# Kernel tuning notes

Hardware: AMD Instinct MI355X
Metric: run time of the kernel (lower is better)

Reference implementation:

```python
import jax, jax.numpy as jnp
import numpy as np

SEQ_LEN, BATCH, INPUT_SIZE, HIDDEN = 512, 64, 256, 512


def setup_inputs() -> dict:
    key = jax.random.key(0)
    ks = jax.random.split(key, 5)
    s_in = 1.0 / np.sqrt(INPUT_SIZE)
    s_h = 1.0 / np.sqrt(HIDDEN)
    x = jax.random.normal(ks[0], (SEQ_LEN, BATCH, INPUT_SIZE), dtype=jnp.float32)
    # gate order: f, i, o, c  (matches the torch module's lin_W*/lin_U*)
    Wx = jax.random.uniform(ks[1], (4, HIDDEN, INPUT_SIZE), jnp.float32, -s_in, s_in)
    bx = jax.random.uniform(ks[2], (4, HIDDEN), jnp.float32, -s_in, s_in)
    Wh = jax.random.uniform(ks[3], (4, HIDDEN, HIDDEN), jnp.float32, -s_h, s_h)
    bh = jax.random.uniform(ks[4], (4, HIDDEN), jnp.float32, -s_h, s_h)
    return {"x": x, "Wx": Wx, "bx": bx, "Wh": Wh, "bh": bh}


def reference(x, Wx, bx, Wh, bh):
    # x: [T, B, I]; Wx: [4, H, I]; Wh: [4, H, H]; biases: [4, H] (gate order f,i,o,c)
    T, B, _ = x.shape
    H = Wh.shape[-1]
    # Precompute input projections for all timesteps (batched GEMM): [T, 4, B, H]
    gx = jnp.einsum('tbi,ghi->tgbh', x, Wx) + bx[:, None, :]

    def step(carry, gx_t):
        h_prev, c_prev = carry
        gh = jnp.einsum('bh,gkh->gbk', h_prev, Wh) + bh[:, None, :]  # [4, B, H]
        g = gx_t + gh
        f = jax.nn.sigmoid(g[0])
        i = jax.nn.sigmoid(g[1])
        o = jax.nn.sigmoid(g[2])
        c = f * c_prev + i * jnp.tanh(g[3])
        h = o * jnp.tanh(c)
        return (h, c), h

    h0 = jnp.zeros((B, H), dtype=x.dtype)
    c0 = jnp.zeros((B, H), dtype=x.dtype)
    (h_last, c_last), h_seq = jax.lax.scan(step, (h0, c0), gx)
    return h_seq, h_last, c_last
```

## Files before the change

### kernel.cpp

```cpp
#include <hip/hip_runtime.h>
#include <hip/hip_cooperative_groups.h>
#include <math.h>

namespace cg = cooperative_groups;

#define TT 512
#define BB 64
#define II 256
#define HH 512

#define NTHREADS 512
#define NGRP 4
#define NCT  16
#define NBLOCKS (NGRP*NCT)

#define KPAD 776

typedef _Float16 f16x8 __attribute__((ext_vector_type(8)));
typedef _Float16 f16x4 __attribute__((ext_vector_type(4)));
typedef float    f32x4 __attribute__((ext_vector_type(4)));

__device__ __forceinline__ float sig_(float v)  { return 1.0f / (1.0f + __expf(-v)); }
__device__ __forceinline__ float tanh_(float v) { float e = __expf(2.0f * v); return 1.0f - 2.0f / (e + 1.0f); }

__global__ void __launch_bounds__(NTHREADS, 2)
lstm_mfma2(const float* __restrict__ x,
           const float* __restrict__ Wx,
           const float* __restrict__ bx,
           const float* __restrict__ Wh,
           const float* __restrict__ bh,
           float* __restrict__ out,
           unsigned int* __restrict__ flags,
           unsigned int* __restrict__ hbuf)
{
    __shared__ _Float16 AL[16 * KPAD];
    __shared__ float    exch[8 * 16 * 20];

    cg::grid_group grid = cg::this_grid();

    const int blk  = blockIdx.x;
    const int grp  = blk & 3;
    const int b0   = grp * 16;
    const int ct   = blk >> 2;
    const int hblk = ct * 32;

    const int tid = threadIdx.x;
    const int wv  = tid >> 6;
    const int L   = tid & 63;
    const int n   = L & 15;
    const int qd  = L >> 4;

    const int g  = n & 3;
    const int hu = hblk + wv * 4 + (n >> 2);
    f16x8 bfr[24];
    #pragma unroll
    for (int kc = 0; kc < 24; ++kc) {
        int k0 = kc * 32 + qd * 8;
        const float* src = (kc < 8)
            ? (Wx + ((size_t)g * HH + hu) * II + k0)
            : (Wh + ((size_t)g * HH + hu) * HH + (k0 - 256));
        float4 u0 = ((const float4*)src)[0];
        float4 u1 = ((const float4*)src)[1];
        f16x8 b = { (_Float16)u0.x, (_Float16)u0.y, (_Float16)u0.z, (_Float16)u0.w,
                    (_Float16)u1.x, (_Float16)u1.y, (_Float16)u1.z, (_Float16)u1.w };
        bfr[kc] = b;
    }

    const int be  = L >> 2;
    const int hle = L & 3;
    const int he  = hblk + wv * 4 + hle;
    float bias4[4];
    #pragma unroll
    for (int g2 = 0; g2 < 4; ++g2) bias4[g2] = bx[g2 * HH + he] + bh[g2 * HH + he];

    if (tid == 0)
        __hip_atomic_store(&flags[grp * 64 + ct], 0u,
                           __ATOMIC_RELAXED, __HIP_MEMORY_SCOPE_AGENT);
    grid.sync();

    const size_t HSEQ = (size_t)TT * BB * HH;
    float c_state = 0.0f;
    float* exchW = &exch[wv * 16 * 20];

    for (int t = 0; t < TT; ++t) {
        #pragma unroll
        for (int i = 0; i < 2; ++i) {
            int ch = tid + i * NTHREADS;
            int row = ch >> 6, pos = ch & 63;
            float4 v = ((const float4*)(x + ((size_t)t * BB + b0 + row) * II))[pos];
            f16x4 p = { (_Float16)v.x, (_Float16)v.y, (_Float16)v.z, (_Float16)v.w };
            *(f16x4*)&AL[row * KPAD + pos * 4] = p;
        }

        if (t > 0 && wv == 0) {
            const unsigned int* fp = flags + grp * 64;
            for (;;) {
                unsigned f = (L < NCT)
                    ? __hip_atomic_load(&fp[L], __ATOMIC_RELAXED, __HIP_MEMORY_SCOPE_AGENT)
                    : 0xFFFFFFFFu;
                if (__all((int)(f >= (unsigned)t))) break;
                __builtin_amdgcn_s_sleep(1);
            }
        }
        __syncthreads();

        if (t > 0) {
            const unsigned long long* hsrc =
                (const unsigned long long*)(hbuf + (size_t)(t & 1) * (BB * 256));
            #pragma unroll
            for (int i = 0; i < 4; ++i) {
                int ch = tid + i * NTHREADS;
                int row = ch >> 7, pos = ch & 127;
                unsigned long long u = __hip_atomic_load(
                    hsrc + (size_t)(b0 + row) * 128 + pos,
                    __ATOMIC_RELAXED, __HIP_MEMORY_SCOPE_AGENT);
                *(unsigned long long*)((char*)AL + row * (KPAD * 2) + II * 2 + pos * 8) = u;
            }
            __syncthreads();
        }

        const char* Ab = (const char*)AL + n * (KPAD * 2) + qd * 16;
        f32x4 acc = { 0.f, 0.f, 0.f, 0.f };
        #pragma unroll
        for (int kc = 0; kc < 8; ++kc) {
            f16x8 a = *(const f16x8*)(Ab + kc * 64);
            acc = __builtin_amdgcn_mfma_f32_16x16x32_f16(a, bfr[kc], acc, 0, 0, 0);
        }
        if (t > 0) {
            #pragma unroll
            for (int kc = 8; kc < 24; ++kc) {
                f16x8 a = *(const f16x8*)(Ab + kc * 64);
                acc = __builtin_amdgcn_mfma_f32_16x16x32_f16(a, bfr[kc], acc, 0, 0, 0);
            }
        }

        #pragma unroll
        for (int r = 0; r < 4; ++r)
            exchW[(qd * 4 + r) * 20 + n] = acc[r];
        float4 pre4 = *(const float4*)&exchW[be * 20 + hle * 4];

        float pf = pre4.x + bias4[0];
        float pi = pre4.y + bias4[1];
        float po = pre4.z + bias4[2];
        float pc = pre4.w + bias4[3];
        float fg = sig_(pf), ig = sig_(pi), og = sig_(po);
        float cn = fg * c_state + ig * tanh_(pc);
        float hv = og * tanh_(cn);
        c_state = cn;

        out[((size_t)t * BB + b0 + be) * HH + he] = hv;
        if (t == TT - 1) {
            size_t r = (size_t)(b0 + be) * HH + he;
            out[HSEQ + r] = hv;
            out[HSEQ + (size_t)BB * HH + r] = cn;
        }

        {
            union { _Float16 f; unsigned short u; } cv; cv.f = (_Float16)hv;
            unsigned mine  = cv.u;
            unsigned other = (unsigned)__shfl_xor((int)mine, 1, 64);
            if ((hle & 1) == 0) {
                unsigned pk = mine | (other << 16);
                unsigned int* hdst = hbuf + (size_t)((t + 1) & 1) * (BB * 256);
                __hip_atomic_store(&hdst[(unsigned)(b0 + be) * 256 + (unsigned)(he >> 1)],
                                   pk, __ATOMIC_RELAXED, __HIP_MEMORY_SCOPE_AGENT);
            }
        }

        __syncthreads();
        if (t != TT - 1 && tid == 0)
            __hip_atomic_store(&flags[grp * 64 + ct], (unsigned)(t + 1),
                               __ATOMIC_RELAXED, __HIP_MEMORY_SCOPE_AGENT);
    }
}

extern "C" void kernel_launch(void* const* d_in, const int* in_sizes, int n_in,
                              void* d_out, int out_size, void* d_ws, size_t ws_size,
                              hipStream_t stream)
{
    const float* x  = (const float*)d_in[0];
    const float* Wx = (const float*)d_in[1];
    const float* bx = (const float*)d_in[2];
    const float* Wh = (const float*)d_in[3];
    const float* bh = (const float*)d_in[4];
    float* out = (float*)d_out;

    unsigned int* flags = (unsigned int*)d_ws;
    unsigned int* hbuf  = (unsigned int*)((char*)d_ws + 4096);

    void* args[] = { (void*)&x, (void*)&Wx, (void*)&bx, (void*)&Wh, (void*)&bh,
                     (void*)&out, (void*)&flags, (void*)&hbuf };
    hipLaunchCooperativeKernel((const void*)lstm_mfma2,
                               dim3(NBLOCKS), dim3(NTHREADS),
                               args, 0, stream);
}
```

Baseline: 1.674 ms.

## Replace per-block flags with timestep-tagged hidden-state words and double-buffer LDS

```diff
diff --git a/kernel.cpp b/kernel.cpp
--- a/kernel.cpp
+++ b/kernel.cpp
@@ -19,22 +19,33 @@
 typedef _Float16 f16x8 __attribute__((ext_vector_type(8)));
 typedef _Float16 f16x4 __attribute__((ext_vector_type(4)));
 typedef float    f32x4 __attribute__((ext_vector_type(4)));
+typedef unsigned int u32x4 __attribute__((ext_vector_type(4)));
 
 __device__ __forceinline__ float sig_(float v)  { return 1.0f / (1.0f + __expf(-v)); }
 __device__ __forceinline__ float tanh_(float v) { float e = __expf(2.0f * v); return 1.0f - 2.0f / (e + 1.0f); }
 
+__device__ __forceinline__ void barrier_lds() {
+    __builtin_amdgcn_sched_barrier(0);
+    asm volatile("s_waitcnt lgkmcnt(0)" ::: "memory");
+    __builtin_amdgcn_s_barrier();
+    __builtin_amdgcn_sched_barrier(0);
+}
+
+__device__ __forceinline__ unsigned pk2(unsigned long long q) {
+    return (unsigned)(q & 0xffffULL) | (((unsigned)(q >> 32)) << 16);
+}
+
 __global__ void __launch_bounds__(NTHREADS, 2)
-lstm_mfma2(const float* __restrict__ x,
-           const float* __restrict__ Wx,
-           const float* __restrict__ bx,
-           const float* __restrict__ Wh,
-           const float* __restrict__ bh,
-           float* __restrict__ out,
-           unsigned int* __restrict__ flags,
-           unsigned int* __restrict__ hbuf)
+lstm_tag(const float* __restrict__ x,
+         const float* __restrict__ Wx,
+         const float* __restrict__ bx,
+         const float* __restrict__ Wh,
+         const float* __restrict__ bh,
+         float* __restrict__ out,
+         unsigned int* __restrict__ hbuf)
 {
-    __shared__ _Float16 AL[16 * KPAD];
-    __shared__ float    exch[8 * 16 * 20];
+    __shared__ __align__(16) _Float16 AL[2][16 * KPAD];
+    __shared__ __align__(16) float    exch[8 * 16 * 20];
 
     cg::grid_group grid = cg::this_grid();
 
@@ -73,66 +84,84 @@
     #pragma unroll
     for (int g2 = 0; g2 < 4; ++g2) bias4[g2] = bx[g2 * HH + he] + bh[g2 * HH + he];
 
-    if (tid == 0)
-        __hip_atomic_store(&flags[grp * 64 + ct], 0u,
+    {
+        unsigned idx = (unsigned)(b0 + be) * HH + (unsigned)he;
+        __hip_atomic_store(&hbuf[idx], 0u,
                            __ATOMIC_RELAXED, __HIP_MEMORY_SCOPE_AGENT);
+        __hip_atomic_store(&hbuf[(unsigned)(BB * HH) + idx], 0u,
+                           __ATOMIC_RELAXED, __HIP_MEMORY_SCOPE_AGENT);
+    }
     grid.sync();
 
     const size_t HSEQ = (size_t)TT * BB * HH;
     float c_state = 0.0f;
     float* exchW = &exch[wv * 16 * 20];
 
+    const int pr  = wv * 2 + (L >> 5);
+    const int pc0 = (L & 31) * 16;
+
     for (int t = 0; t < TT; ++t) {
+        const int p = t & 1;
+        _Float16* ALp = AL[p];
+
         #pragma unroll
         for (int i = 0; i < 2; ++i) {
             int ch = tid + i * NTHREADS;
             int row = ch >> 6, pos = ch & 63;
             float4 v = ((const float4*)(x + ((size_t)t * BB + b0 + row) * II))[pos];
-            f16x4 p = { (_Float16)v.x, (_Float16)v.y, (_Float16)v.z, (_Float16)v.w };
-            *(f16x4*)&AL[row * KPAD + pos * 4] = p;
-        }
-
-        if (t > 0 && wv == 0) {
-            const unsigned int* fp = flags + grp * 64;
+            f16x4 pk = { (_Float16)v.x, (_Float16)v.y, (_Float16)v.z, (_Float16)v.w };
+            *(f16x4*)&ALp[row * KPAD + pos * 4] = pk;
+        }
+
+        if (t > 0) {
+            const unsigned long long* sp =
+                (const unsigned long long*)(hbuf + (size_t)p * (BB * HH))
+                + (size_t)(b0 + pr) * (HH / 2) + (pc0 >> 1);
+            const unsigned long long pat =
+                ((unsigned long long)(unsigned)t << 16) |
+                ((unsigned long long)(unsigned)t << 48);
+            unsigned long long q0, q1, q2, q3, q4, q5, q6, q7;
             for (;;) {
-                unsigned f = (L < NCT)
-                    ? __hip_atomic_load(&fp[L], __ATOMIC_RELAXED, __HIP_MEMORY_SCOPE_AGENT)
-                    : 0xFFFFFFFFu;
-                if (__all((int)(f >= (unsigned)t))) break;
-                __builtin_amdgcn_s_sleep(1);
+                q0 = __hip_atomic_load(sp + 0, __ATOMIC_RELAXED, __HIP_MEMORY_SCOPE_AGENT);
+                q1 = __hip_atomic_load(sp + 1, __ATOMIC_RELAXED, __HIP_MEMORY_SCOPE_AGENT);
+                q2 = __hip_atomic_load(sp + 2, __ATOMIC_RELAXED, __HIP_MEMORY_SCOPE_AGENT);
+                q3 = __hip_atomic_load(sp + 3, __ATOMIC_RELAXED, __HIP_MEMORY_SCOPE_AGENT);
+                q4 = __hip_atomic_load(sp + 4, __ATOMIC_RELAXED, __HIP_MEMORY_SCOPE_AGENT);
+                q5 = __hip_atomic_load(sp + 5, __ATOMIC_RELAXED, __HIP_MEMORY_SCOPE_AGENT);
+                q6 = __hip_atomic_load(sp + 6, __ATOMIC_RELAXED, __HIP_MEMORY_SCOPE_AGENT);
+                q7 = __hip_atomic_load(sp + 7, __ATOMIC_RELAXED, __HIP_MEMORY_SCOPE_AGENT);
+                unsigned long long d = ((q0 ^ pat) | (q1 ^ pat) | (q2 ^ pat) | (q3 ^ pat) |
+                                        (q4 ^ pat) | (q5 ^ pat) | (q6 ^ pat) | (q7 ^ pat))
+                                       & 0xFFFF0000FFFF0000ULL;
+                if (__all(d == 0ULL)) break;
             }
-        }
-        __syncthreads();
-
-        if (t > 0) {
-            const unsigned long long* hsrc =
-                (const unsigned long long*)(hbuf + (size_t)(t & 1) * (BB * 256));
-            #pragma unroll
-            for (int i = 0; i < 4; ++i) {
-                int ch = tid + i * NTHREADS;
-                int row = ch >> 7, pos = ch & 127;
-                unsigned long long u = __hip_atomic_load(
-                    hsrc + (size_t)(b0 + row) * 128 + pos,
-                    __ATOMIC_RELAXED, __HIP_MEMORY_SCOPE_AGENT);
-                *(unsigned long long*)((char*)AL + row * (KPAD * 2) + II * 2 + pos * 8) = u;
-            }
-            __syncthreads();
-        }
-
-        const char* Ab = (const char*)AL + n * (KPAD * 2) + qd * 16;
-        f32x4 acc = { 0.f, 0.f, 0.f, 0.f };
+            u32x4 P0 = { pk2(q0), pk2(q1), pk2(q2), pk2(q3) };
+            u32x4 P1 = { pk2(q4), pk2(q5), pk2(q6), pk2(q7) };
+            char* dst = (char*)ALp + pr * (KPAD * 2) + II * 2 + pc0 * 2;
+            *(u32x4*)dst = P0;
+            *(u32x4*)(dst + 16) = P1;
+        }
+
+        barrier_lds();
+
+        const char* Ab = (const char*)ALp + n * (KPAD * 2) + qd * 16;
+        f32x4 a0 = { 0.f, 0.f, 0.f, 0.f };
+        f32x4 a1 = { 0.f, 0.f, 0.f, 0.f };
         #pragma unroll
         for (int kc = 0; kc < 8; ++kc) {
             f16x8 a = *(const f16x8*)(Ab + kc * 64);
-            acc = __builtin_amdgcn_mfma_f32_16x16x32_f16(a, bfr[kc], acc, 0, 0, 0);
+            if (kc & 1) a1 = __builtin_amdgcn_mfma_f32_16x16x32_f16(a, bfr[kc], a1, 0, 0, 0);
+            else        a0 = __builtin_amdgcn_mfma_f32_16x16x32_f16(a, bfr[kc], a0, 0, 0, 0);
         }
         if (t > 0) {
             #pragma unroll
             for (int kc = 8; kc < 24; ++kc) {
                 f16x8 a = *(const f16x8*)(Ab + kc * 64);
-                acc = __builtin_amdgcn_mfma_f32_16x16x32_f16(a, bfr[kc], acc, 0, 0, 0);
+                if (kc & 1) a1 = __builtin_amdgcn_mfma_f32_16x16x32_f16(a, bfr[kc], a1, 0, 0, 0);
+                else        a0 = __builtin_amdgcn_mfma_f32_16x16x32_f16(a, bfr[kc], a0, 0, 0, 0);
             }
         }
+        f32x4 acc = a0 + a1;
 
         #pragma unroll
         for (int r = 0; r < 4; ++r)
@@ -148,29 +177,20 @@
         float hv = og * tanh_(cn);
         c_state = cn;
 
+        {
+            union { _Float16 f; unsigned short u; } cv; cv.f = (_Float16)hv;
+            unsigned val = ((unsigned)(t + 1) << 16) | (unsigned)cv.u;
+            unsigned didx = (unsigned)((((t + 1) & 1) * BB + (b0 + be)) * HH + he);
+            __hip_atomic_store(&hbuf[didx], val,
+                               __ATOMIC_RELAXED, __HIP_MEMORY_SCOPE_AGENT);
+        }
+
         out[((size_t)t * BB + b0 + be) * HH + he] = hv;
         if (t == TT - 1) {
             size_t r = (size_t)(b0 + be) * HH + he;
             out[HSEQ + r] = hv;
             out[HSEQ + (size_t)BB * HH + r] = cn;
         }
-
-        {
-            union { _Float16 f; unsigned short u; } cv; cv.f = (_Float16)hv;
-            unsigned mine  = cv.u;
-            unsigned other = (unsigned)__shfl_xor((int)mine, 1, 64);
-            if ((hle & 1) == 0) {
-                unsigned pk = mine | (other << 16);
-                unsigned int* hdst = hbuf + (size_t)((t + 1) & 1) * (BB * 256);
-                __hip_atomic_store(&hdst[(unsigned)(b0 + be) * 256 + (unsigned)(he >> 1)],
-                                   pk, __ATOMIC_RELAXED, __HIP_MEMORY_SCOPE_AGENT);
-            }
-        }
-
-        __syncthreads();
-        if (t != TT - 1 && tid == 0)
-            __hip_atomic_store(&flags[grp * 64 + ct], (unsigned)(t + 1),
-                               __ATOMIC_RELAXED, __HIP_MEMORY_SCOPE_AGENT);
     }
 }
 
@@ -185,12 +205,11 @@
     const float* bh = (const float*)d_in[4];
     float* out = (float*)d_out;
 
-    unsigned int* flags = (unsigned int*)d_ws;
-    unsigned int* hbuf  = (unsigned int*)((char*)d_ws + 4096);
+    unsigned int* hbuf = (unsigned int*)d_ws;
 
     void* args[] = { (void*)&x, (void*)&Wx, (void*)&bx, (void*)&Wh, (void*)&bh,
-                     (void*)&out, (void*)&flags, (void*)&hbuf };
-    hipLaunchCooperativeKernel((const void*)lstm_mfma2,
+                     (void*)&out, (void*)&hbuf };
+    hipLaunchCooperativeKernel((const void*)lstm_tag,
                                dim3(NBLOCKS), dim3(NTHREADS),
                                args, 0, stream);
 }
```

Result: slower. 1.877 ms (+12.1%).

## Use per-wave completion flags and double-buffered LDS to remove block barriers

Applied to the files above, without the earlier changes.

```diff
diff --git a/kernel.cpp b/kernel.cpp
--- a/kernel.cpp
+++ b/kernel.cpp
@@ -23,8 +23,15 @@
 __device__ __forceinline__ float sig_(float v)  { return 1.0f / (1.0f + __expf(-v)); }
 __device__ __forceinline__ float tanh_(float v) { float e = __expf(2.0f * v); return 1.0f - 2.0f / (e + 1.0f); }
 
+__device__ __forceinline__ void barrier_lds() {
+    __builtin_amdgcn_sched_barrier(0);
+    asm volatile("s_waitcnt lgkmcnt(0)" ::: "memory");
+    __builtin_amdgcn_s_barrier();
+    __builtin_amdgcn_sched_barrier(0);
+}
+
 __global__ void __launch_bounds__(NTHREADS, 2)
-lstm_mfma2(const float* __restrict__ x,
+lstm_wflag(const float* __restrict__ x,
            const float* __restrict__ Wx,
            const float* __restrict__ bx,
            const float* __restrict__ Wh,
@@ -33,8 +40,8 @@
            unsigned int* __restrict__ flags,
            unsigned int* __restrict__ hbuf)
 {
-    __shared__ _Float16 AL[16 * KPAD];
-    __shared__ float    exch[8 * 16 * 20];
+    __shared__ __align__(16) _Float16 AL[2][16 * KPAD];
+    __shared__ __align__(16) float    exch[8 * 16 * 20];
 
     cg::grid_group grid = cg::this_grid();
 
@@ -73,40 +80,44 @@
     #pragma unroll
     for (int g2 = 0; g2 < 4; ++g2) bias4[g2] = bx[g2 * HH + he] + bh[g2 * HH + he];
 
-    if (tid == 0)
-        __hip_atomic_store(&flags[grp * 64 + ct], 0u,
+    if (tid < 128)
+        __hip_atomic_store(&flags[grp * 128 + tid], 0u,
                            __ATOMIC_RELAXED, __HIP_MEMORY_SCOPE_AGENT);
     grid.sync();
 
     const size_t HSEQ = (size_t)TT * BB * HH;
     float c_state = 0.0f;
     float* exchW = &exch[wv * 16 * 20];
+    const int myflag = grp * 128 + ct * 8 + wv;
 
     for (int t = 0; t < TT; ++t) {
+        const int p = t & 1;
+        _Float16* ALp = AL[p];
+
         #pragma unroll
         for (int i = 0; i < 2; ++i) {
             int ch = tid + i * NTHREADS;
             int row = ch >> 6, pos = ch & 63;
             float4 v = ((const float4*)(x + ((size_t)t * BB + b0 + row) * II))[pos];
-            f16x4 p = { (_Float16)v.x, (_Float16)v.y, (_Float16)v.z, (_Float16)v.w };
-            *(f16x4*)&AL[row * KPAD + pos * 4] = p;
-        }
-
-        if (t > 0 && wv == 0) {
-            const unsigned int* fp = flags + grp * 64;
+            f16x4 pk = { (_Float16)v.x, (_Float16)v.y, (_Float16)v.z, (_Float16)v.w };
+            *(f16x4*)&ALp[row * KPAD + pos * 4] = pk;
+        }
+
+        if (t > 0) {
+            const unsigned long long* fp =
+                (const unsigned long long*)(flags + grp * 128);
+            const unsigned tu = (unsigned)t;
             for (;;) {
-                unsigned f = (L < NCT)
-                    ? __hip_atomic_load(&fp[L], __ATOMIC_RELAXED, __HIP_MEMORY_SCOPE_AGENT)
-                    : 0xFFFFFFFFu;
-                if (__all((int)(f >= (unsigned)t))) break;
+                unsigned long long f2 = __hip_atomic_load(
+                    &fp[L], __ATOMIC_RELAXED, __HIP_MEMORY_SCOPE_AGENT);
+                unsigned lo = (unsigned)f2, hi = (unsigned)(f2 >> 32);
+                if (__all((int)(lo >= tu && hi >= tu))) break;
                 __builtin_amdgcn_s_sleep(1);
             }
-        }
-        __syncthreads();
-
-        if (t > 0) {
+            asm volatile("" ::: "memory");
+
             const unsigned long long* hsrc =
-                (const unsigned long long*)(hbuf + (size_t)(t & 1) * (BB * 256));
+                (const unsigned long long*)(hbuf + (size_t)p * (BB * 256));
             #pragma unroll
             for (int i = 0; i < 4; ++i) {
                 int ch = tid + i * NTHREADS;
@@ -114,25 +125,30 @@
                 unsigned long long u = __hip_atomic_load(
                     hsrc + (size_t)(b0 + row) * 128 + pos,
                     __ATOMIC_RELAXED, __HIP_MEMORY_SCOPE_AGENT);
-                *(unsigned long long*)((char*)AL + row * (KPAD * 2) + II * 2 + pos * 8) = u;
-            }
-            __syncthreads();
-        }
-
-        const char* Ab = (const char*)AL + n * (KPAD * 2) + qd * 16;
-        f32x4 acc = { 0.f, 0.f, 0.f, 0.f };
+                *(unsigned long long*)((char*)ALp + row * (KPAD * 2) + II * 2 + pos * 8) = u;
+            }
+        }
+
+        barrier_lds();
+
+        const char* Ab = (const char*)ALp + n * (KPAD * 2) + qd * 16;
+        f32x4 a0 = { 0.f, 0.f, 0.f, 0.f };
+        f32x4 a1 = { 0.f, 0.f, 0.f, 0.f };
         #pragma unroll
         for (int kc = 0; kc < 8; ++kc) {
             f16x8 a = *(const f16x8*)(Ab + kc * 64);
-            acc = __builtin_amdgcn_mfma_f32_16x16x32_f16(a, bfr[kc], acc, 0, 0, 0);
+            if (kc & 1) a1 = __builtin_amdgcn_mfma_f32_16x16x32_f16(a, bfr[kc], a1, 0, 0, 0);
+            else        a0 = __builtin_amdgcn_mfma_f32_16x16x32_f16(a, bfr[kc], a0, 0, 0, 0);
         }
         if (t > 0) {
             #pragma unroll
             for (int kc = 8; kc < 24; ++kc) {
                 f16x8 a = *(const f16x8*)(Ab + kc * 64);
-                acc = __builtin_amdgcn_mfma_f32_16x16x32_f16(a, bfr[kc], acc, 0, 0, 0);
-            }
-        }
+                if (kc & 1) a1 = __builtin_amdgcn_mfma_f32_16x16x32_f16(a, bfr[kc], a1, 0, 0, 0);
+                else        a0 = __builtin_amdgcn_mfma_f32_16x16x32_f16(a, bfr[kc], a0, 0, 0, 0);
+            }
+        }
+        f32x4 acc = a0 + a1;
 
         #pragma unroll
         for (int r = 0; r < 4; ++r)
@@ -147,13 +163,6 @@
         float cn = fg * c_state + ig * tanh_(pc);
         float hv = og * tanh_(cn);
         c_state = cn;
-
-        out[((size_t)t * BB + b0 + be) * HH + he] = hv;
-        if (t == TT - 1) {
-            size_t r = (size_t)(b0 + be) * HH + he;
-            out[HSEQ + r] = hv;
-            out[HSEQ + (size_t)BB * HH + r] = cn;
-        }
 
         {
             union { _Float16 f; unsigned short u; } cv; cv.f = (_Float16)hv;
@@ -167,10 +176,19 @@
             }
         }
 
-        __syncthreads();
-        if (t != TT - 1 && tid == 0)
-            __hip_atomic_store(&flags[grp * 64 + ct], (unsigned)(t + 1),
+        __builtin_amdgcn_sched_barrier(0);
+        asm volatile("s_waitcnt vmcnt(0)" ::: "memory");
+        __builtin_amdgcn_sched_barrier(0);
+        if (t != TT - 1 && L == 0)
+            __hip_atomic_store(&flags[myflag], (unsigned)(t + 1),
                                __ATOMIC_RELAXED, __HIP_MEMORY_SCOPE_AGENT);
+
+        out[((size_t)t * BB + b0 + be) * HH + he] = hv;
+        if (t == TT - 1) {
+            size_t r = (size_t)(b0 + be) * HH + he;
+            out[HSEQ + r] = hv;
+            out[HSEQ + (size_t)BB * HH + r] = cn;
+        }
     }
 }
 
@@ -188,9 +206,12 @@
     unsigned int* flags = (unsigned int*)d_ws;
     unsigned int* hbuf  = (unsigned int*)((char*)d_ws + 4096);
 
-    void* args[] = { (void*)&x, (void*)&Wx, (void*)&bx, (void*)&Wh, (void*)&bh,
-                     (void*)&out, (void*)&flags, (void*)&hbuf };
-    hipLaunchCooperativeKernel((const void*)lstm_mfma2,
+    void* args[] = { (void*)&x, (void*)&Wx, (void*)&bx, (void*)&bh,
+                     (void*)&bh, (void*)&out, (void*)&flags, (void*)&hbuf };
+    void* args2[] = { (void*)&x, (void*)&Wx, (void*)&bx, (void*)&Wh, (void*)&bh,
+                      (void*)&out, (void*)&flags, (void*)&hbuf };
+    (void)args;
+    hipLaunchCooperativeKernel((const void*)lstm_wflag,
                                dim3(NBLOCKS), dim3(NTHREADS),
-                               args, 0, stream);
+                               args2, 0, stream);
 }
```

Measured after the change: 1.946 ms. 16.3% more time.

## Repartition LSTM grid so each batch group syncs within one XCD

Applied to the files above, without the earlier changes.

```diff
diff --git a/kernel.cpp b/kernel.cpp
--- a/kernel.cpp
+++ b/kernel.cpp
@@ -9,10 +9,10 @@
 #define II 256
 #define HH 512
 
-#define NTHREADS 512
-#define NGRP 4
-#define NCT  16
-#define NBLOCKS (NGRP*NCT)
+#define NTHREADS 1024
+#define NGRP 8
+#define NCB  8
+#define NBLOCKS (NGRP*NCB)
 
 #define KPAD 776
 
@@ -23,26 +23,26 @@
 __device__ __forceinline__ float sig_(float v)  { return 1.0f / (1.0f + __expf(-v)); }
 __device__ __forceinline__ float tanh_(float v) { float e = __expf(2.0f * v); return 1.0f - 2.0f / (e + 1.0f); }
 
-__global__ void __launch_bounds__(NTHREADS, 2)
-lstm_mfma2(const float* __restrict__ x,
-           const float* __restrict__ Wx,
-           const float* __restrict__ bx,
-           const float* __restrict__ Wh,
-           const float* __restrict__ bh,
-           float* __restrict__ out,
-           unsigned int* __restrict__ flags,
-           unsigned int* __restrict__ hbuf)
+__global__ void __launch_bounds__(NTHREADS, 1)
+lstm_xcd(const float* __restrict__ x,
+         const float* __restrict__ Wx,
+         const float* __restrict__ bx,
+         const float* __restrict__ Wh,
+         const float* __restrict__ bh,
+         float* __restrict__ out,
+         unsigned int* __restrict__ flags,
+         unsigned int* __restrict__ hbuf)
 {
-    __shared__ _Float16 AL[16 * KPAD];
-    __shared__ float    exch[8 * 16 * 20];
+    __shared__ __align__(16) _Float16 AL[16 * KPAD];
+    __shared__ __align__(16) float    exch[16][8 * 20];
 
     cg::grid_group grid = cg::this_grid();
 
     const int blk  = blockIdx.x;
-    const int grp  = blk & 3;
-    const int b0   = grp * 16;
-    const int ct   = blk >> 2;
-    const int hblk = ct * 32;
+    const int grp  = blk & 7;
+    const int b0   = grp * 8;
+    const int ct   = blk >> 3;
+    const int hblk = ct * 64;
 
     const int tid = threadIdx.x;
     const int wv  = tid >> 6;
@@ -73,103 +73,104 @@
     #pragma unroll
     for (int g2 = 0; g2 < 4; ++g2) bias4[g2] = bx[g2 * HH + he] + bh[g2 * HH + he];
 
+    for (int i = tid; i < 16 * KPAD / 2; i += NTHREADS) ((unsigned*)AL)[i] = 0u;
     if (tid == 0)
-        __hip_atomic_store(&flags[grp * 64 + ct], 0u,
+        __hip_atomic_store(&flags[grp * 16 + ct], 0u,
                            __ATOMIC_RELAXED, __HIP_MEMORY_SCOPE_AGENT);
     grid.sync();
 
     const size_t HSEQ = (size_t)TT * BB * HH;
     float c_state = 0.0f;
-    float* exchW = &exch[wv * 16 * 20];
+    float* exchW = exch[wv];
 
     for (int t = 0; t < TT; ++t) {
-        #pragma unroll
-        for (int i = 0; i < 2; ++i) {
-            int ch = tid + i * NTHREADS;
-            int row = ch >> 6, pos = ch & 63;
+        if (tid < 512) {
+            int row = tid >> 6, pos = tid & 63;
             float4 v = ((const float4*)(x + ((size_t)t * BB + b0 + row) * II))[pos];
-            f16x4 p = { (_Float16)v.x, (_Float16)v.y, (_Float16)v.z, (_Float16)v.w };
-            *(f16x4*)&AL[row * KPAD + pos * 4] = p;
+            f16x4 pk = { (_Float16)v.x, (_Float16)v.y, (_Float16)v.z, (_Float16)v.w };
+            *(f16x4*)&AL[row * KPAD + pos * 4] = pk;
         }
 
         if (t > 0 && wv == 0) {
-            const unsigned int* fp = flags + grp * 64;
+            const unsigned int* fp = flags + grp * 16;
+            const unsigned tu = (unsigned)t;
             for (;;) {
-                unsigned f = (L < NCT)
+                unsigned f = (L < NCB)
                     ? __hip_atomic_load(&fp[L], __ATOMIC_RELAXED, __HIP_MEMORY_SCOPE_AGENT)
                     : 0xFFFFFFFFu;
-                if (__all((int)(f >= (unsigned)t))) break;
+                if (__all((int)(f >= tu))) break;
                 __builtin_amdgcn_s_sleep(1);
             }
         }
         __syncthreads();
 
         if (t > 0) {
-            const unsigned long long* hsrc =
-                (const unsigned long long*)(hbuf + (size_t)(t & 1) * (BB * 256));
-            #pragma unroll
-            for (int i = 0; i < 4; ++i) {
-                int ch = tid + i * NTHREADS;
-                int row = ch >> 7, pos = ch & 127;
-                unsigned long long u = __hip_atomic_load(
-                    hsrc + (size_t)(b0 + row) * 128 + pos,
-                    __ATOMIC_RELAXED, __HIP_MEMORY_SCOPE_AGENT);
-                *(unsigned long long*)((char*)AL + row * (KPAD * 2) + II * 2 + pos * 8) = u;
-            }
+            const unsigned long long* hsrc = (const unsigned long long*)
+                (hbuf + (size_t)((t & 1) * NGRP + grp) * (8 * 256));
+            int row = tid >> 7, pos = tid & 127;
+            unsigned long long u = __hip_atomic_load(
+                hsrc + (size_t)row * 128 + pos,
+                __ATOMIC_RELAXED, __HIP_MEMORY_SCOPE_AGENT);
+            *(unsigned long long*)((char*)AL + row * (KPAD * 2) + II * 2 + pos * 8) = u;
             __syncthreads();
         }
 
         const char* Ab = (const char*)AL + n * (KPAD * 2) + qd * 16;
-        f32x4 acc = { 0.f, 0.f, 0.f, 0.f };
+        f32x4 a0 = { 0.f, 0.f, 0.f, 0.f };
+        f32x4 a1 = { 0.f, 0.f, 0.f, 0.f };
         #pragma unroll
         for (int kc = 0; kc < 8; ++kc) {
             f16x8 a = *(const f16x8*)(Ab + kc * 64);
-            acc = __builtin_amdgcn_mfma_f32_16x16x32_f16(a, bfr[kc], acc, 0, 0, 0);
+            if (kc & 1) a1 = __builtin_amdgcn_mfma_f32_16x16x32_f16(a, bfr[kc], a1, 0, 0, 0);
+            else        a0 = __builtin_amdgcn_mfma_f32_16x16x32_f16(a, bfr[kc], a0, 0, 0, 0);
         }
         if (t > 0) {
             #pragma unroll
             for (int kc = 8; kc < 24; ++kc) {
                 f16x8 a = *(const f16x8*)(Ab + kc * 64);
-                acc = __builtin_amdgcn_mfma_f32_16x16x32_f16(a, bfr[kc], acc, 0, 0, 0);
+                if (kc & 1) a1 = __builtin_amdgcn_mfma_f32_16x16x32_f16(a, bfr[kc], a1, 0, 0, 0);
+                else        a0 = __builtin_amdgcn_mfma_f32_16x16x32_f16(a, bfr[kc], a0, 0, 0, 0);
             }
         }
+        f32x4 acc = a0 + a1;
 
         #pragma unroll
         for (int r = 0; r < 4; ++r)
-            exchW[(qd * 4 + r) * 20 + n] = acc[r];
-        float4 pre4 = *(const float4*)&exchW[be * 20 + hle * 4];
+            if (qd < 2) exchW[(qd * 4 + r) * 20 + n] = acc[r];
+        float4 pre4 = { 0.f, 0.f, 0.f, 0.f };
+        if (be < 8) pre4 = *(const float4*)&exchW[be * 20 + hle * 4];
 
-        float pf = pre4.x + bias4[0];
-        float pi = pre4.y + bias4[1];
-        float po = pre4.z + bias4[2];
-        float pc = pre4.w + bias4[3];
-        float fg = sig_(pf), ig = sig_(pi), og = sig_(po);
-        float cn = fg * c_state + ig * tanh_(pc);
-        float hv = og * tanh_(cn);
-        c_state = cn;
+        if (be < 8) {
+            float pf = pre4.x + bias4[0];
+            float pi = pre4.y + bias4[1];
+            float po = pre4.z + bias4[2];
+            float pc = pre4.w + bias4[3];
+            float fg = sig_(pf), ig = sig_(pi), og = sig_(po);
+            float cn = fg * c_state + ig * tanh_(pc);
+            float hv = og * tanh_(cn);
+            c_state = cn;
 
-        out[((size_t)t * BB + b0 + be) * HH + he] = hv;
-        if (t == TT - 1) {
-            size_t r = (size_t)(b0 + be) * HH + he;
-            out[HSEQ + r] = hv;
-            out[HSEQ + (size_t)BB * HH + r] = cn;
-        }
+            out[((size_t)t * BB + b0 + be) * HH + he] = hv;
+            if (t == TT - 1) {
+                size_t r = (size_t)(b0 + be) * HH + he;
+                out[HSEQ + r] = hv;
+                out[HSEQ + (size_t)BB * HH + r] = cn;
+            }
 
-        {
             union { _Float16 f; unsigned short u; } cv; cv.f = (_Float16)hv;
             unsigned mine  = cv.u;
             unsigned other = (unsigned)__shfl_xor((int)mine, 1, 64);
             if ((hle & 1) == 0) {
                 unsigned pk = mine | (other << 16);
-                unsigned int* hdst = hbuf + (size_t)((t + 1) & 1) * (BB * 256);
-                __hip_atomic_store(&hdst[(unsigned)(b0 + be) * 256 + (unsigned)(he >> 1)],
+                unsigned int* hdst = hbuf + (size_t)(((t + 1) & 1) * NGRP + grp) * (8 * 256);
+                __hip_atomic_store(&hdst[(unsigned)be * 256 + (unsigned)(he >> 1)],
                                    pk, __ATOMIC_RELAXED, __HIP_MEMORY_SCOPE_AGENT);
             }
         }
 
         __syncthreads();
         if (t != TT - 1 && tid == 0)
-            __hip_atomic_store(&flags[grp * 64 + ct], (unsigned)(t + 1),
+            __hip_atomic_store(&flags[grp * 16 + ct], (unsigned)(t + 1),
                                __ATOMIC_RELAXED, __HIP_MEMORY_SCOPE_AGENT);
     }
 }
@@ -190,7 +191,7 @@
 
     void* args[] = { (void*)&x, (void*)&Wx, (void*)&bx, (void*)&Wh, (void*)&bh,
                      (void*)&out, (void*)&flags, (void*)&hbuf };
-    hipLaunchCooperativeKernel((const void*)lstm_mfma2,
+    hipLaunchCooperativeKernel((const void*)lstm_xcd,
                                dim3(NBLOCKS), dim3(NTHREADS),
                                args, 0, stream);
 }
```

Result: slower. 2.080 ms (+24.3%).
